# Performance work log

Hardware: AMD Instinct MI355X
Metric: run time of the kernel (lower is better)

## Reference

```python
import jax, jax.numpy as jnp
import numpy as np

N_NODES = 50000
N_EDGES = 800000
IN_C, HID_C, OUT_C, HEADS = 128, 32, 64, 8
NEG_SLOPE = 0.2


def gat_layer(x, src, dst, W, a_src, a_dst, bias, concat, num_nodes):
    # W: [F_in, H*C]; a_src, a_dst: [H, C]; bias: [H*C] or [C]
    H, C = a_src.shape
    h = (x @ W).reshape(num_nodes, H, C)                      # [N,H,C]
    e_src = (h * a_src).sum(-1)                               # [N,H]
    e_dst = (h * a_dst).sum(-1)                               # [N,H]
    e = jax.nn.leaky_relu(e_src[src] + e_dst[dst], NEG_SLOPE) # [E,H]
    # segment softmax over incoming edges of each destination node
    m = jax.ops.segment_max(e, dst, num_segments=num_nodes)   # [N,H]
    ex = jnp.exp(e - m[dst])
    den = jax.ops.segment_sum(ex, dst, num_segments=num_nodes)
    alpha = ex / (den[dst] + 1e-16)                           # [E,H]
    out = jax.ops.segment_sum(h[src] * alpha[..., None], dst, num_segments=num_nodes)  # [N,H,C]
    out = out.reshape(num_nodes, H * C) if concat else out.mean(axis=1)
    return out + bias


def setup_inputs() -> dict:
    key = jax.random.key(0)
    ks = jax.random.split(key, 10)
    x = jax.random.normal(ks[0], (N_NODES, IN_C), dtype=jnp.float32)
    edge_index = jax.random.randint(ks[1], (2, N_EDGES), 0, N_NODES, dtype=jnp.int64)
    s1 = (2.0 / (IN_C + HID_C * HEADS)) ** 0.5
    s2 = (2.0 / (HID_C * HEADS + OUT_C)) ** 0.5
    return {
        "x": x,
        "edge_index": edge_index,
        "W1": jax.random.normal(ks[2], (IN_C, HEADS * HID_C), dtype=jnp.float32) * s1,
        "a_src1": jax.random.normal(ks[3], (HEADS, HID_C), dtype=jnp.float32) * 0.1,
        "a_dst1": jax.random.normal(ks[4], (HEADS, HID_C), dtype=jnp.float32) * 0.1,
        "b1": jnp.zeros((HEADS * HID_C,), dtype=jnp.float32),
        "W2": jax.random.normal(ks[5], (HEADS * HID_C, OUT_C), dtype=jnp.float32) * s2,
        "a_src2": jax.random.normal(ks[6], (1, OUT_C), dtype=jnp.float32) * 0.1,
        "a_dst2": jax.random.normal(ks[7], (1, OUT_C), dtype=jnp.float32) * 0.1,
        "b2": jnp.zeros((OUT_C,), dtype=jnp.float32),
    }


def reference(x, edge_index, W1, a_src1, a_dst1, b1, W2, a_src2, a_dst2, b2):
    # add self-loops (PyG GATConv default)
    loops = jnp.arange(N_NODES, dtype=edge_index.dtype)
    src = jnp.concatenate([edge_index[0], loops])
    dst = jnp.concatenate([edge_index[1], loops])
    # dropout layers are identity in eval mode
    h = gat_layer(x, src, dst, W1, a_src1, a_dst1, b1, True, N_NODES)
    h = jax.nn.elu(h)
    out = gat_layer(h, src, dst, W2, a_src2, a_dst2, b2, False, N_NODES)
    return out
```

## Files before the change

kernel.cpp:

```cpp
#include <hip/hip_runtime.h>
#include <math.h>

#define N_NODES 50000
#define N_EDGES 800000
#define E_TOT   850000
#define IN_C    128
#define HID_C   32
#define OUT_C   64
#define HEADS   8
#define F1      256
#define PAD     64
#define NDUMMY  1024
#define G1_BLOCKS 3125
#define CSR_BLOCKS 782

typedef __bf16 bf16x8 __attribute__((ext_vector_type(8)));
typedef float  f32x4  __attribute__((ext_vector_type(4)));
typedef float  f32x2  __attribute__((ext_vector_type(2)));
typedef unsigned short us8 __attribute__((ext_vector_type(8)));

__device__ __forceinline__ unsigned short f2b(float f) {
    unsigned u = __float_as_uint(f);
    u += 0x7FFF + ((u >> 16) & 1);
    return (unsigned short)(u >> 16);
}
__device__ __forceinline__ float b2f(unsigned short b) {
    return __uint_as_float(((unsigned)b) << 16);
}
__device__ __forceinline__ float blo(unsigned u) { return __uint_as_float(u << 16); }
__device__ __forceinline__ float bhi(unsigned u) { return __uint_as_float(u & 0xffff0000u); }
__device__ __forceinline__ f32x2 up2(unsigned u) {
    f32x2 r; r.x = blo(u); r.y = bhi(u); return r;
}

__global__ void convert_w(const float* __restrict__ W1, const float* __restrict__ W2,
                          unsigned short* __restrict__ W1t, unsigned short* __restrict__ W2t,
                          int* __restrict__ deg, int* __restrict__ ssrc) {
    int gid = blockIdx.x * 256 + threadIdx.x;
    if (gid < N_NODES) {
        deg[gid] = 1;
        ssrc[gid * PAD] = gid;
    } else if (gid < N_NODES + NDUMMY) {
        deg[gid] = 0;
    }
    if (gid < 256 * 128) {
        int n = gid >> 7, k = gid & 127;
        W1t[gid] = f2b(W1[k * F1 + n]);
    } else if (gid < 256 * 128 + 64 * 256) {
        int o = gid - 256 * 128;
        int n = o >> 8, k = o & 255;
        W2t[o] = f2b(W2[k * OUT_C + n]);
    }
}

__global__ void csr_build(const int* __restrict__ ei, int* __restrict__ deg,
                          int* __restrict__ ssrc) {
    int e0 = blockIdx.x * 1024 + threadIdx.x;
    int s[4], d[4], p[4];
#pragma unroll
    for (int j = 0; j < 4; j++) {
        int e = e0 + j * 256;
        int le = (e < N_EDGES) ? e : (N_EDGES - 1);
        int es = ei[le];
        int ed = ei[N_EDGES + le];
        s[j] = es;
        d[j] = (e < N_EDGES) ? ed : (N_NODES + (e - N_EDGES));
    }
#pragma unroll
    for (int j = 0; j < 4; j++) p[j] = atomicAdd(&deg[d[j]], 1);
#pragma unroll
    for (int j = 0; j < 4; j++) ssrc[d[j] * PAD + p[j]] = s[j];
}

__global__ __launch_bounds__(256) void gemm1_mfma(const float* __restrict__ x,
                                                  const unsigned short* __restrict__ W1t,
                                                  const float* __restrict__ a_src,
                                                  const float* __restrict__ a_dst,
                                                  unsigned short* __restrict__ h1b,
                                                  float* __restrict__ e_src,
                                                  float* __restrict__ e_dst) {
    const int t = threadIdx.x;
    const int wave = t >> 6, lane = t & 63;
    const int mlane = lane & 15, quad = lane >> 4;
    const int row0 = blockIdx.x * 16;
    const int col0 = wave * 64;
    const float* xr = x + (size_t)(row0 + mlane) * IN_C;
    bf16x8 afr[4];
#pragma unroll
    for (int kc = 0; kc < 4; kc++) {
        float4 f0 = *(const float4*)&xr[kc * 32 + quad * 8];
        float4 f1 = *(const float4*)&xr[kc * 32 + quad * 8 + 4];
        us8 u;
        u[0] = f2b(f0.x); u[1] = f2b(f0.y); u[2] = f2b(f0.z); u[3] = f2b(f0.w);
        u[4] = f2b(f1.x); u[5] = f2b(f1.y); u[6] = f2b(f1.z); u[7] = f2b(f1.w);
        afr[kc] = __builtin_bit_cast(bf16x8, u);
    }
    f32x4 c[4];
#pragma unroll
    for (int nt = 0; nt < 4; nt++) c[nt] = (f32x4){0.f, 0.f, 0.f, 0.f};
#pragma unroll
    for (int kc = 0; kc < 4; kc++) {
#pragma unroll
        for (int nt = 0; nt < 4; nt++) {
            int col = col0 + nt * 16 + mlane;
            uint4 bw = *(const uint4*)&W1t[(size_t)col * IN_C + kc * 32 + quad * 8];
            bf16x8 b = __builtin_bit_cast(bf16x8, bw);
            c[nt] = __builtin_amdgcn_mfma_f32_16x16x32_bf16(afr[kc], b, c[nt], 0, 0, 0);
        }
    }
#pragma unroll
    for (int nt = 0; nt < 4; nt++) {
#pragma unroll
        for (int r = 0; r < 4; r++) {
            int gr = row0 + quad * 4 + r;
            h1b[(size_t)gr * F1 + col0 + nt * 16 + mlane] = f2b(c[nt][r]);
        }
    }
    float asA0 = a_src[col0 + mlane],      asA1 = a_src[col0 + 16 + mlane];
    float asB0 = a_src[col0 + 32 + mlane], asB1 = a_src[col0 + 48 + mlane];
    float adA0 = a_dst[col0 + mlane],      adA1 = a_dst[col0 + 16 + mlane];
    float adB0 = a_dst[col0 + 32 + mlane], adB1 = a_dst[col0 + 48 + mlane];
#pragma unroll
    for (int r = 0; r < 4; r++) {
        float psA = c[0][r] * asA0 + c[1][r] * asA1;
        float pdA = c[0][r] * adA0 + c[1][r] * adA1;
        float psB = c[2][r] * asB0 + c[3][r] * asB1;
        float pdB = c[2][r] * adB0 + c[3][r] * adB1;
#pragma unroll
        for (int off = 1; off < 16; off <<= 1) {
            psA += __shfl_xor(psA, off, 64);
            pdA += __shfl_xor(pdA, off, 64);
            psB += __shfl_xor(psB, off, 64);
            pdB += __shfl_xor(pdB, off, 64);
        }
        if (mlane == 0) {
            int gr = row0 + quad * 4 + r;
            e_src[gr * HEADS + wave * 2]     = psA;
            e_src[gr * HEADS + wave * 2 + 1] = psB;
            e_dst[gr * HEADS + wave * 2]     = pdA;
            e_dst[gr * HEADS + wave * 2 + 1] = pdB;
        }
    }
}

__global__ __launch_bounds__(256) void agg1s(const unsigned short* __restrict__ h1b,
                                             const float* __restrict__ e_src,
                                             const float* __restrict__ e_dst,
                                             const int* __restrict__ deg,
                                             const int* __restrict__ ssrc,
                                             const float* __restrict__ b1,
                                             unsigned short* __restrict__ hhb) {
    int v = (blockIdx.x * 256 + threadIdx.x) >> 6;
    int lane = threadIdx.x & 63;
    int half = lane >> 5, l32 = lane & 31;
    int c0 = l32 * 8, h_acc = l32 >> 2;
    int c2 = c0 << 1;
    int h_exp = l32 & 7, j_exp = l32 >> 3;
    const char* h1c = (const char*)h1b;
    const char* esc = (const char*)e_src;
    int d = deg[v];
    int beg = v * PAD;
    int s_all = ssrc[beg + lane];
    float edh = e_dst[v * HEADS + h_exp];
    f32x2 acc[4];
#pragma unroll
    for (int k = 0; k < 4; k++) acc[k] = (f32x2){0.f, 0.f};
    float den = 0.f;
    int dm1 = d - 1;
    for (int k16 = 0; k16 < d; k16 += 16) {
        int slotA = k16 + half + 2 * j_exp;
        int slotB = slotA + 8;
        int sA = __shfl(s_all, (slotA < dm1 ? slotA : dm1), 64);
        int sB = __shfl(s_all, (slotB < dm1 ? slotB : dm1), 64);
        float eA = *(const float*)(esc + ((sA << 5) + (h_exp << 2))) + edh;
        float eB = *(const float*)(esc + ((sB << 5) + (h_exp << 2))) + edh;
        eA = fmaxf(eA, 0.2f * eA);
        eB = fmaxf(eB, 0.2f * eB);
        float wA = (slotA < d) ? __expf(eA) : 0.f;
        float wB = (slotB < d) ? __expf(eB) : 0.f;
        int s_j[8];
#pragma unroll
        for (int j = 0; j < 8; j++) {
            int slot = k16 + half + 2 * j;
            s_j[j] = __shfl(s_all, (slot < dm1 ? slot : dm1), 64);
        }
        float w_j[8];
#pragma unroll
        for (int j = 0; j < 4; j++) {
            w_j[j]     = __shfl(wA, (j << 3) | h_acc, 32);
            w_j[j + 4] = __shfl(wB, (j << 3) | h_acc, 32);
        }
        uint4 r[8];
#pragma unroll
        for (int j = 0; j < 8; j++)
            r[j] = *(const uint4*)(h1c + (((unsigned)s_j[j] << 9) + c2));
#pragma unroll
        for (int j = 0; j < 8; j++) {
            den += w_j[j];
            acc[0] += w_j[j] * up2(r[j].x);
            acc[1] += w_j[j] * up2(r[j].y);
            acc[2] += w_j[j] * up2(r[j].z);
            acc[3] += w_j[j] * up2(r[j].w);
        }
    }
    den += __shfl_xor(den, 32, 64);
#pragma unroll
    for (int k = 0; k < 4; k++) {
        acc[k].x += __shfl_xor(acc[k].x, 32, 64);
        acc[k].y += __shfl_xor(acc[k].y, 32, 64);
    }
    if (half == 0) {
        float dinv = 1.f / (den + 1e-16f);
        us8 o;
#pragma unroll
        for (int k = 0; k < 4; k++) {
            float v0 = acc[k].x * dinv + b1[c0 + 2 * k];
            float v1 = acc[k].y * dinv + b1[c0 + 2 * k + 1];
            v0 = (v0 > 0.f) ? v0 : (__expf(v0) - 1.f);
            v1 = (v1 > 0.f) ? v1 : (__expf(v1) - 1.f);
            o[2 * k]     = f2b(v0);
            o[2 * k + 1] = f2b(v1);
        }
        *(us8*)&hhb[(size_t)v * F1 + c0] = o;
    }
}

__global__ __launch_bounds__(256) void gemm2_mfma(const unsigned short* __restrict__ hhb,
                                                  const unsigned short* __restrict__ W2t,
                                                  const float* __restrict__ a_src,
                                                  const float* __restrict__ a_dst,
                                                  unsigned short* __restrict__ h2b,
                                                  float* __restrict__ e_src,
                                                  float* __restrict__ e_dst) {
    const int t = threadIdx.x;
    const int wave = t >> 6, lane = t & 63;
    const int mlane = lane & 15, quad = lane >> 4;
    const int row0 = blockIdx.x * 64 + wave * 16;
    int arow = row0 + mlane;
    if (arow >= N_NODES) arow = N_NODES - 1;
    const unsigned short* ar = hhb + (size_t)arow * F1;
    f32x4 c[4];
#pragma unroll
    for (int nt = 0; nt < 4; nt++) c[nt] = (f32x4){0.f, 0.f, 0.f, 0.f};
#pragma unroll
    for (int kc = 0; kc < 8; kc++) {
        uint4 aw = *(const uint4*)&ar[kc * 32 + quad * 8];
        bf16x8 a = __builtin_bit_cast(bf16x8, aw);
#pragma unroll
        for (int nt = 0; nt < 4; nt++) {
            int col = nt * 16 + mlane;
            uint4 bw = *(const uint4*)&W2t[(size_t)col * F1 + kc * 32 + quad * 8];
            bf16x8 b = __builtin_bit_cast(bf16x8, bw);
            c[nt] = __builtin_amdgcn_mfma_f32_16x16x32_bf16(a, b, c[nt], 0, 0, 0);
        }
    }
#pragma unroll
    for (int nt = 0; nt < 4; nt++) {
#pragma unroll
        for (int r = 0; r < 4; r++) {
            int gr = row0 + quad * 4 + r;
            if (gr < N_NODES)
                h2b[(size_t)gr * OUT_C + nt * 16 + mlane] = f2b(c[nt][r]);
        }
    }
    float as0 = a_src[mlane],      as1 = a_src[16 + mlane];
    float as2 = a_src[32 + mlane], as3 = a_src[48 + mlane];
    float ad0 = a_dst[mlane],      ad1 = a_dst[16 + mlane];
    float ad2 = a_dst[32 + mlane], ad3 = a_dst[48 + mlane];
#pragma unroll
    for (int r = 0; r < 4; r++) {
        float ps = c[0][r] * as0 + c[1][r] * as1 + c[2][r] * as2 + c[3][r] * as3;
        float pd = c[0][r] * ad0 + c[1][r] * ad1 + c[2][r] * ad2 + c[3][r] * ad3;
#pragma unroll
        for (int off = 1; off < 16; off <<= 1) {
            ps += __shfl_xor(ps, off, 64);
            pd += __shfl_xor(pd, off, 64);
        }
        int gr = row0 + quad * 4 + r;
        if (mlane == 0 && gr < N_NODES) { e_src[gr] = ps; e_dst[gr] = pd; }
    }
}

__global__ __launch_bounds__(256) void agg2s(const unsigned short* __restrict__ h2b,
                                             const float* __restrict__ e_src,
                                             const float* __restrict__ e_dst,
                                             const int* __restrict__ deg,
                                             const int* __restrict__ ssrc,
                                             const float* __restrict__ b2,
                                             float* __restrict__ out) {
    int v = (blockIdx.x * 256 + threadIdx.x) >> 6;
    int lane = threadIdx.x & 63;
    int d = deg[v], beg = v * PAD, dm1 = d - 1;
    float ed = e_dst[v];
    int g = lane >> 3, l8 = lane & 7;
    int c0 = l8 * 8;
    int c2 = c0 << 1;
    const char* h2c = (const char*)h2b;
    const char* esc = (const char*)e_src;
    int s_raw = ssrc[beg + lane];
    int s_cl = s_raw < 0 ? 0 : (s_raw > N_NODES - 1 ? N_NODES - 1 : s_raw);
    float e_own = *(const float*)(esc + (s_cl << 2)) + ed;
    e_own = fmaxf(e_own, 0.2f * e_own);
    float w_own = (lane < d) ? __expf(e_own) : 0.f;
    f32x2 acc[4];
#pragma unroll
    for (int k = 0; k < 4; k++) acc[k] = (f32x2){0.f, 0.f};
    float den = 0.f;
    for (int k16 = 0; k16 < d; k16 += 16) {
        int slot0 = k16 + g, slot1 = slot0 + 8;
        int t0 = slot0 < dm1 ? slot0 : dm1;
        int t1 = slot1 < dm1 ? slot1 : dm1;
        int s0 = __shfl(s_cl, t0, 64);
        int s1 = __shfl(s_cl, t1, 64);
        float w0 = __shfl(w_own, t0, 64); w0 = (slot0 < d) ? w0 : 0.f;
        float w1 = __shfl(w_own, t1, 64); w1 = (slot1 < d) ? w1 : 0.f;
        den += w0 + w1;
        uint4 r0 = *(const uint4*)(h2c + ((s0 << 7) + c2));
        uint4 r1 = *(const uint4*)(h2c + ((s1 << 7) + c2));
        acc[0] += w0 * up2(r0.x) + w1 * up2(r1.x);
        acc[1] += w0 * up2(r0.y) + w1 * up2(r1.y);
        acc[2] += w0 * up2(r0.z) + w1 * up2(r1.z);
        acc[3] += w0 * up2(r0.w) + w1 * up2(r1.w);
    }
    den += __shfl_xor(den, 8, 64);
    den += __shfl_xor(den, 16, 64);
    den += __shfl_xor(den, 32, 64);
#pragma unroll
    for (int k = 0; k < 4; k++) {
        acc[k].x += __shfl_xor(acc[k].x, 8, 64);
        acc[k].y += __shfl_xor(acc[k].y, 8, 64);
        acc[k].x += __shfl_xor(acc[k].x, 16, 64);
        acc[k].y += __shfl_xor(acc[k].y, 16, 64);
        acc[k].x += __shfl_xor(acc[k].x, 32, 64);
        acc[k].y += __shfl_xor(acc[k].y, 32, 64);
    }
    if (g == 0) {
        float dinv = 1.f / (den + 1e-16f);
        float4 lo, hi;
        lo.x = acc[0].x * dinv + b2[c0 + 0]; lo.y = acc[0].y * dinv + b2[c0 + 1];
        lo.z = acc[1].x * dinv + b2[c0 + 2]; lo.w = acc[1].y * dinv + b2[c0 + 3];
        hi.x = acc[2].x * dinv + b2[c0 + 4]; hi.y = acc[2].y * dinv + b2[c0 + 5];
        hi.z = acc[3].x * dinv + b2[c0 + 6]; hi.w = acc[3].y * dinv + b2[c0 + 7];
        *(float4*)&out[(size_t)v * OUT_C + c0] = lo;
        *(float4*)&out[(size_t)v * OUT_C + c0 + 4] = hi;
    }
}

extern "C" void kernel_launch(void* const* d_in, const int* in_sizes, int n_in,
                              void* d_out, int out_size, void* d_ws, size_t ws_size,
                              hipStream_t stream) {
    const float* x      = (const float*)d_in[0];
    const int*   ei     = (const int*)d_in[1];
    const float* W1     = (const float*)d_in[2];
    const float* a_src1 = (const float*)d_in[3];
    const float* a_dst1 = (const float*)d_in[4];
    const float* b1     = (const float*)d_in[5];
    const float* W2     = (const float*)d_in[6];
    const float* a_src2 = (const float*)d_in[7];
    const float* a_dst2 = (const float*)d_in[8];
    const float* b2     = (const float*)d_in[9];
    float* out = (float*)d_out;

    char* ws = (char*)d_ws;
    size_t off = 0;
    auto alloc = [&](size_t bytes) { void* p = ws + off; off = (off + bytes + 255) & ~(size_t)255; return p; };
    unsigned short* h1b = (unsigned short*)alloc((size_t)N_NODES * F1 * 2);
    unsigned short* hhb = (unsigned short*)alloc((size_t)N_NODES * F1 * 2);
    unsigned short* h2b = (unsigned short*)alloc((size_t)N_NODES * OUT_C * 2);
    unsigned short* W1t = (unsigned short*)alloc((size_t)256 * 128 * 2);
    unsigned short* W2t = (unsigned short*)alloc((size_t)64 * 256 * 2);
    float* e_src1 = (float*)alloc((size_t)N_NODES * HEADS * 4);
    float* e_dst1 = (float*)alloc((size_t)N_NODES * HEADS * 4);
    float* e_src2 = (float*)alloc((size_t)N_NODES * 4);
    float* e_dst2 = (float*)alloc((size_t)N_NODES * 4);
    int*   deg    = (int*)alloc((size_t)(N_NODES + NDUMMY) * 4);
    int*   ssrc   = (int*)alloc((size_t)(N_NODES + NDUMMY) * PAD * 4);
    (void)ws_size; (void)n_in; (void)in_sizes; (void)out_size;

    const int g2_blocks  = (N_NODES + 63) / 64;
    const int node_waves = (N_NODES + 3) / 4;

    convert_w<<<200, 256, 0, stream>>>(W1, W2, W1t, W2t, deg, ssrc);
    csr_build<<<CSR_BLOCKS, 256, 0, stream>>>(ei, deg, ssrc);
    gemm1_mfma<<<G1_BLOCKS, 256, 0, stream>>>(x, W1t, a_src1, a_dst1, h1b, e_src1, e_dst1);
    agg1s<<<node_waves, 256, 0, stream>>>(h1b, e_src1, e_dst1, deg, ssrc, b1, hhb);
    gemm2_mfma<<<g2_blocks, 256, 0, stream>>>(hhb, W2t, a_src2, a_dst2, h2b, e_src2, e_dst2);
    agg2s<<<node_waves, 256, 0, stream>>>(h2b, e_src2, e_dst2, deg, ssrc, b2, out);
}
```

Before: 291.3 us.

## Fuse layer-2 linear transform into layer-1 aggregation kernel via LDS

The layer-1 aggregation kernel now keeps each node's ELU output row in shared memory and immediately multiplies it by W2 (repacked as bf16 pairs) with scalar FMAs. It also computes the layer-2 attention scores, so the separate MFMA GEMM2 kernel and the 25MB hhb intermediate buffer are removed. This saves a full write and read of the hidden activations plus one launch. In exchange, each wave now does a 256x64 dot product without tensor cores and reads W2 from cache per node. It also adds a __syncthreads inside the aggregation kernel.

```diff
diff --git a/kernel.cpp b/kernel.cpp
--- a/kernel.cpp
+++ b/kernel.cpp
@@ -34,7 +34,7 @@
 }
 
 __global__ void convert_w(const float* __restrict__ W1, const float* __restrict__ W2,
-                          unsigned short* __restrict__ W1t, unsigned short* __restrict__ W2t,
+                          unsigned short* __restrict__ W1t, unsigned* __restrict__ W2p,
                           int* __restrict__ deg, int* __restrict__ ssrc) {
     int gid = blockIdx.x * 256 + threadIdx.x;
     if (gid < N_NODES) {
@@ -46,10 +46,12 @@
     if (gid < 256 * 128) {
         int n = gid >> 7, k = gid & 127;
         W1t[gid] = f2b(W1[k * F1 + n]);
-    } else if (gid < 256 * 128 + 64 * 256) {
+    } else if (gid < 256 * 128 + 128 * 64) {
         int o = gid - 256 * 128;
-        int n = o >> 8, k = o & 255;
-        W2t[o] = f2b(W2[k * OUT_C + n]);
+        int kk = o >> 6, col = o & 63;
+        unsigned lo = f2b(W2[(2 * kk) * OUT_C + col]);
+        unsigned hi = f2b(W2[(2 * kk + 1) * OUT_C + col]);
+        W2p[o] = lo | (hi << 16);
     }
 }
 
@@ -143,14 +145,21 @@
     }
 }
 
-__global__ __launch_bounds__(256) void agg1s(const unsigned short* __restrict__ h1b,
+__global__ __launch_bounds__(256) void agg1f(const unsigned short* __restrict__ h1b,
                                              const float* __restrict__ e_src,
                                              const float* __restrict__ e_dst,
                                              const int* __restrict__ deg,
                                              const int* __restrict__ ssrc,
                                              const float* __restrict__ b1,
-                                             unsigned short* __restrict__ hhb) {
-    int v = (blockIdx.x * 256 + threadIdx.x) >> 6;
+                                             const unsigned* __restrict__ W2p,
+                                             const float* __restrict__ a_src2,
+                                             const float* __restrict__ a_dst2,
+                                             unsigned short* __restrict__ h2b,
+                                             float* __restrict__ e_src2,
+                                             float* __restrict__ e_dst2) {
+    __shared__ unsigned hh_lds[4][128];
+    int wave = threadIdx.x >> 6;
+    int v = blockIdx.x * 4 + wave;
     int lane = threadIdx.x & 63;
     int half = lane >> 5, l32 = lane & 31;
     int c0 = l32 * 8, h_acc = l32 >> 2;
@@ -221,64 +230,33 @@
             o[2 * k]     = f2b(v0);
             o[2 * k + 1] = f2b(v1);
         }
-        *(us8*)&hhb[(size_t)v * F1 + c0] = o;
-    }
-}
-
-__global__ __launch_bounds__(256) void gemm2_mfma(const unsigned short* __restrict__ hhb,
-                                                  const unsigned short* __restrict__ W2t,
-                                                  const float* __restrict__ a_src,
-                                                  const float* __restrict__ a_dst,
-                                                  unsigned short* __restrict__ h2b,
-                                                  float* __restrict__ e_src,
-                                                  float* __restrict__ e_dst) {
-    const int t = threadIdx.x;
-    const int wave = t >> 6, lane = t & 63;
-    const int mlane = lane & 15, quad = lane >> 4;
-    const int row0 = blockIdx.x * 64 + wave * 16;
-    int arow = row0 + mlane;
-    if (arow >= N_NODES) arow = N_NODES - 1;
-    const unsigned short* ar = hhb + (size_t)arow * F1;
-    f32x4 c[4];
-#pragma unroll
-    for (int nt = 0; nt < 4; nt++) c[nt] = (f32x4){0.f, 0.f, 0.f, 0.f};
-#pragma unroll
-    for (int kc = 0; kc < 8; kc++) {
-        uint4 aw = *(const uint4*)&ar[kc * 32 + quad * 8];
-        bf16x8 a = __builtin_bit_cast(bf16x8, aw);
-#pragma unroll
-        for (int nt = 0; nt < 4; nt++) {
-            int col = nt * 16 + mlane;
-            uint4 bw = *(const uint4*)&W2t[(size_t)col * F1 + kc * 32 + quad * 8];
-            bf16x8 b = __builtin_bit_cast(bf16x8, bw);
-            c[nt] = __builtin_amdgcn_mfma_f32_16x16x32_bf16(a, b, c[nt], 0, 0, 0);
-        }
-    }
-#pragma unroll
-    for (int nt = 0; nt < 4; nt++) {
-#pragma unroll
-        for (int r = 0; r < 4; r++) {
-            int gr = row0 + quad * 4 + r;
-            if (gr < N_NODES)
-                h2b[(size_t)gr * OUT_C + nt * 16 + mlane] = f2b(c[nt][r]);
-        }
-    }
-    float as0 = a_src[mlane],      as1 = a_src[16 + mlane];
-    float as2 = a_src[32 + mlane], as3 = a_src[48 + mlane];
-    float ad0 = a_dst[mlane],      ad1 = a_dst[16 + mlane];
-    float ad2 = a_dst[32 + mlane], ad3 = a_dst[48 + mlane];
-#pragma unroll
-    for (int r = 0; r < 4; r++) {
-        float ps = c[0][r] * as0 + c[1][r] * as1 + c[2][r] * as2 + c[3][r] * as3;
-        float pd = c[0][r] * ad0 + c[1][r] * ad1 + c[2][r] * ad2 + c[3][r] * ad3;
-#pragma unroll
-        for (int off = 1; off < 16; off <<= 1) {
-            ps += __shfl_xor(ps, off, 64);
-            pd += __shfl_xor(pd, off, 64);
-        }
-        int gr = row0 + quad * 4 + r;
-        if (mlane == 0 && gr < N_NODES) { e_src[gr] = ps; e_dst[gr] = pd; }
-    }
+        *(uint4*)&hh_lds[wave][l32 * 4] = __builtin_bit_cast(uint4, o);
+    }
+    __syncthreads();
+    const unsigned* hw = hh_lds[wave];
+    f32x2 macc = (f32x2){0.f, 0.f};
+#pragma unroll 4
+    for (int kk = 0; kk < 128; kk += 4) {
+        uint4 hv = *(const uint4*)&hw[kk];
+        unsigned w0 = W2p[(kk + 0) * 64 + lane];
+        unsigned w1 = W2p[(kk + 1) * 64 + lane];
+        unsigned w2 = W2p[(kk + 2) * 64 + lane];
+        unsigned w3 = W2p[(kk + 3) * 64 + lane];
+        macc += up2(hv.x) * up2(w0);
+        macc += up2(hv.y) * up2(w1);
+        macc += up2(hv.z) * up2(w2);
+        macc += up2(hv.w) * up2(w3);
+    }
+    float val = macc.x + macc.y;
+    h2b[(size_t)v * OUT_C + lane] = f2b(val);
+    float ps = val * a_src2[lane];
+    float pd = val * a_dst2[lane];
+#pragma unroll
+    for (int off = 1; off < 64; off <<= 1) {
+        ps += __shfl_xor(ps, off, 64);
+        pd += __shfl_xor(pd, off, 64);
+    }
+    if (lane == 0) { e_src2[v] = ps; e_dst2[v] = pd; }
 }
 
 __global__ __launch_bounds__(256) void agg2s(const unsigned short* __restrict__ h2b,
@@ -365,10 +343,9 @@
     size_t off = 0;
     auto alloc = [&](size_t bytes) { void* p = ws + off; off = (off + bytes + 255) & ~(size_t)255; return p; };
     unsigned short* h1b = (unsigned short*)alloc((size_t)N_NODES * F1 * 2);
-    unsigned short* hhb = (unsigned short*)alloc((size_t)N_NODES * F1 * 2);
     unsigned short* h2b = (unsigned short*)alloc((size_t)N_NODES * OUT_C * 2);
     unsigned short* W1t = (unsigned short*)alloc((size_t)256 * 128 * 2);
-    unsigned short* W2t = (unsigned short*)alloc((size_t)64 * 256 * 2);
+    unsigned*       W2p = (unsigned*)alloc((size_t)128 * 64 * 4);
     float* e_src1 = (float*)alloc((size_t)N_NODES * HEADS * 4);
     float* e_dst1 = (float*)alloc((size_t)N_NODES * HEADS * 4);
     float* e_src2 = (float*)alloc((size_t)N_NODES * 4);
@@ -377,13 +354,12 @@
     int*   ssrc   = (int*)alloc((size_t)(N_NODES + NDUMMY) * PAD * 4);
     (void)ws_size; (void)n_in; (void)in_sizes; (void)out_size;
 
-    const int g2_blocks  = (N_NODES + 63) / 64;
     const int node_waves = (N_NODES + 3) / 4;
 
-    convert_w<<<200, 256, 0, stream>>>(W1, W2, W1t, W2t, deg, ssrc);
+    convert_w<<<200, 256, 0, stream>>>(W1, W2, W1t, W2p, deg, ssrc);
     csr_build<<<CSR_BLOCKS, 256, 0, stream>>>(ei, deg, ssrc);
     gemm1_mfma<<<G1_BLOCKS, 256, 0, stream>>>(x, W1t, a_src1, a_dst1, h1b, e_src1, e_dst1);
-    agg1s<<<node_waves, 256, 0, stream>>>(h1b, e_src1, e_dst1, deg, ssrc, b1, hhb);
-    gemm2_mfma<<<g2_blocks, 256, 0, stream>>>(hhb, W2t, a_src2, a_dst2, h2b, e_src2, e_dst2);
+    agg1f<<<node_waves, 256, 0, stream>>>(h1b, e_src1, e_dst1, deg, ssrc, b1,
+                                          W2p, a_src2, a_dst2, h2b, e_src2, e_dst2);
     agg2s<<<node_waves, 256, 0, stream>>>(h2b, e_src2, e_dst2, deg, ssrc, b2, out);
 }
```

After: 316.1 us. 8.5% more time.

## Fuse layer-2 projection GEMM into layer-1 aggregation via shared memory

Applied to the files above, without the earlier changes.

The layer-1 aggregation kernel now writes its ELU'd bf16 output row into LDS instead of global memory. Each 4-node block then runs the 256x64 MFMA projection and the attention-logit reductions itself. This removes the 25.6 MB hhb round trip and one kernel launch. In exchange, each wave computes a 16-row MFMA tile of which only 4 rows are distinct nodes, W2 is reloaded per block, and a block-wide barrier now couples the four waves' variable-degree work.

```diff
diff --git a/kernel.cpp b/kernel.cpp
--- a/kernel.cpp
+++ b/kernel.cpp
@@ -143,14 +143,21 @@
     }
 }
 
-__global__ __launch_bounds__(256) void agg1s(const unsigned short* __restrict__ h1b,
+__global__ __launch_bounds__(256) void agg1f(const unsigned short* __restrict__ h1b,
                                              const float* __restrict__ e_src,
                                              const float* __restrict__ e_dst,
                                              const int* __restrict__ deg,
                                              const int* __restrict__ ssrc,
                                              const float* __restrict__ b1,
-                                             unsigned short* __restrict__ hhb) {
-    int v = (blockIdx.x * 256 + threadIdx.x) >> 6;
+                                             const unsigned short* __restrict__ W2t,
+                                             const float* __restrict__ a_src2,
+                                             const float* __restrict__ a_dst2,
+                                             unsigned short* __restrict__ h2b,
+                                             float* __restrict__ e_src2,
+                                             float* __restrict__ e_dst2) {
+    __shared__ unsigned hh_lds[4][128];
+    int wave = threadIdx.x >> 6;
+    int v = blockIdx.x * 4 + wave;
     int lane = threadIdx.x & 63;
     int half = lane >> 5, l32 = lane & 31;
     int c0 = l32 * 8, h_acc = l32 >> 2;
@@ -221,64 +228,47 @@
             o[2 * k]     = f2b(v0);
             o[2 * k + 1] = f2b(v1);
         }
-        *(us8*)&hhb[(size_t)v * F1 + c0] = o;
-    }
-}
-
-__global__ __launch_bounds__(256) void gemm2_mfma(const unsigned short* __restrict__ hhb,
-                                                  const unsigned short* __restrict__ W2t,
-                                                  const float* __restrict__ a_src,
-                                                  const float* __restrict__ a_dst,
-                                                  unsigned short* __restrict__ h2b,
-                                                  float* __restrict__ e_src,
-                                                  float* __restrict__ e_dst) {
-    const int t = threadIdx.x;
-    const int wave = t >> 6, lane = t & 63;
+        *(uint4*)&hh_lds[wave][l32 * 4] = __builtin_bit_cast(uint4, o);
+    }
+    __syncthreads();
     const int mlane = lane & 15, quad = lane >> 4;
-    const int row0 = blockIdx.x * 64 + wave * 16;
-    int arow = row0 + mlane;
-    if (arow >= N_NODES) arow = N_NODES - 1;
-    const unsigned short* ar = hhb + (size_t)arow * F1;
-    f32x4 c[4];
-#pragma unroll
-    for (int nt = 0; nt < 4; nt++) c[nt] = (f32x4){0.f, 0.f, 0.f, 0.f};
+    const unsigned short* hrow = (const unsigned short*)hh_lds[mlane & 3];
+    f32x4 cc[4];
+#pragma unroll
+    for (int nt = 0; nt < 4; nt++) cc[nt] = (f32x4){0.f, 0.f, 0.f, 0.f};
 #pragma unroll
     for (int kc = 0; kc < 8; kc++) {
-        uint4 aw = *(const uint4*)&ar[kc * 32 + quad * 8];
+        uint4 aw = *(const uint4*)&hrow[kc * 32 + quad * 8];
         bf16x8 a = __builtin_bit_cast(bf16x8, aw);
 #pragma unroll
         for (int nt = 0; nt < 4; nt++) {
             int col = nt * 16 + mlane;
             uint4 bw = *(const uint4*)&W2t[(size_t)col * F1 + kc * 32 + quad * 8];
             bf16x8 b = __builtin_bit_cast(bf16x8, bw);
-            c[nt] = __builtin_amdgcn_mfma_f32_16x16x32_bf16(a, b, c[nt], 0, 0, 0);
-        }
-    }
+            cc[nt] = __builtin_amdgcn_mfma_f32_16x16x32_bf16(a, b, cc[nt], 0, 0, 0);
+        }
+    }
+    float val[4];
 #pragma unroll
     for (int nt = 0; nt < 4; nt++) {
-#pragma unroll
-        for (int r = 0; r < 4; r++) {
-            int gr = row0 + quad * 4 + r;
-            if (gr < N_NODES)
-                h2b[(size_t)gr * OUT_C + nt * 16 + mlane] = f2b(c[nt][r]);
-        }
-    }
-    float as0 = a_src[mlane],      as1 = a_src[16 + mlane];
-    float as2 = a_src[32 + mlane], as3 = a_src[48 + mlane];
-    float ad0 = a_dst[mlane],      ad1 = a_dst[16 + mlane];
-    float ad2 = a_dst[32 + mlane], ad3 = a_dst[48 + mlane];
-#pragma unroll
-    for (int r = 0; r < 4; r++) {
-        float ps = c[0][r] * as0 + c[1][r] * as1 + c[2][r] * as2 + c[3][r] * as3;
-        float pd = c[0][r] * ad0 + c[1][r] * ad1 + c[2][r] * ad2 + c[3][r] * ad3;
-#pragma unroll
-        for (int off = 1; off < 16; off <<= 1) {
-            ps += __shfl_xor(ps, off, 64);
-            pd += __shfl_xor(pd, off, 64);
-        }
-        int gr = row0 + quad * 4 + r;
-        if (mlane == 0 && gr < N_NODES) { e_src[gr] = ps; e_dst[gr] = pd; }
-    }
+        float t0 = (wave & 1) ? cc[nt][1] : cc[nt][0];
+        float t1 = (wave & 1) ? cc[nt][3] : cc[nt][2];
+        val[nt] = (wave & 2) ? t1 : t0;
+    }
+    float ps = 0.f, pd = 0.f;
+#pragma unroll
+    for (int nt = 0; nt < 4; nt++) {
+        int col = nt * 16 + mlane;
+        if (quad == 0) h2b[(size_t)v * OUT_C + col] = f2b(val[nt]);
+        ps += val[nt] * a_src2[col];
+        pd += val[nt] * a_dst2[col];
+    }
+#pragma unroll
+    for (int off = 1; off < 16; off <<= 1) {
+        ps += __shfl_xor(ps, off, 64);
+        pd += __shfl_xor(pd, off, 64);
+    }
+    if (lane == 0) { e_src2[v] = ps; e_dst2[v] = pd; }
 }
 
 __global__ __launch_bounds__(256) void agg2s(const unsigned short* __restrict__ h2b,
@@ -365,7 +355,6 @@
     size_t off = 0;
     auto alloc = [&](size_t bytes) { void* p = ws + off; off = (off + bytes + 255) & ~(size_t)255; return p; };
     unsigned short* h1b = (unsigned short*)alloc((size_t)N_NODES * F1 * 2);
-    unsigned short* hhb = (unsigned short*)alloc((size_t)N_NODES * F1 * 2);
     unsigned short* h2b = (unsigned short*)alloc((size_t)N_NODES * OUT_C * 2);
     unsigned short* W1t = (unsigned short*)alloc((size_t)256 * 128 * 2);
     unsigned short* W2t = (unsigned short*)alloc((size_t)64 * 256 * 2);
@@ -377,13 +366,12 @@
     int*   ssrc   = (int*)alloc((size_t)(N_NODES + NDUMMY) * PAD * 4);
     (void)ws_size; (void)n_in; (void)in_sizes; (void)out_size;
 
-    const int g2_blocks  = (N_NODES + 63) / 64;
     const int node_waves = (N_NODES + 3) / 4;
 
     convert_w<<<200, 256, 0, stream>>>(W1, W2, W1t, W2t, deg, ssrc);
     csr_build<<<CSR_BLOCKS, 256, 0, stream>>>(ei, deg, ssrc);
     gemm1_mfma<<<G1_BLOCKS, 256, 0, stream>>>(x, W1t, a_src1, a_dst1, h1b, e_src1, e_dst1);
-    agg1s<<<node_waves, 256, 0, stream>>>(h1b, e_src1, e_dst1, deg, ssrc, b1, hhb);
-    gemm2_mfma<<<g2_blocks, 256, 0, stream>>>(hhb, W2t, a_src2, a_dst2, h2b, e_src2, e_dst2);
+    agg1f<<<node_waves, 256, 0, stream>>>(h1b, e_src1, e_dst1, deg, ssrc, b1,
+                                          W2t, a_src2, a_dst2, h2b, e_src2, e_dst2);
     agg2s<<<node_waves, 256, 0, stream>>>(h2b, e_src2, e_dst2, deg, ssrc, b2, out);
 }
```

After: 429.7 us. +47.5%, slower.

## Fold layer-2 attention projections into agg1 and restructure gemm2 tiling

Applied to the files above, without the earlier changes.

Precomputes W2·a_src2 and W2·a_dst2 once, then computes the layer-2 attention logits inside agg1s from the fp32 ELU outputs, which removes that reduction from gemm2. gemm2 is reorganised so each block handles 16 rows staged through shared memory, with each wave producing one 16-column slice. This gives more, smaller blocks. The logits now come from fp32 activations instead of bf16-rounded GEMM outputs, so numerics shift slightly.

```diff
diff --git a/kernel.cpp b/kernel.cpp
--- a/kernel.cpp
+++ b/kernel.cpp
@@ -34,7 +34,9 @@
 }
 
 __global__ void convert_w(const float* __restrict__ W1, const float* __restrict__ W2,
+                          const float* __restrict__ a_src2, const float* __restrict__ a_dst2,
                           unsigned short* __restrict__ W1t, unsigned short* __restrict__ W2t,
+                          float* __restrict__ w2s, float* __restrict__ w2d,
                           int* __restrict__ deg, int* __restrict__ ssrc) {
     int gid = blockIdx.x * 256 + threadIdx.x;
     if (gid < N_NODES) {
@@ -42,6 +44,15 @@
         ssrc[gid * PAD] = gid;
     } else if (gid < N_NODES + NDUMMY) {
         deg[gid] = 0;
+    }
+    if (gid < 256) {
+        float s = 0.f, dd = 0.f;
+        for (int c = 0; c < OUT_C; c++) {
+            float w = W2[gid * OUT_C + c];
+            s  += w * a_src2[c];
+            dd += w * a_dst2[c];
+        }
+        w2s[gid] = s; w2d[gid] = dd;
     }
     if (gid < 256 * 128) {
         int n = gid >> 7, k = gid & 127;
@@ -149,7 +160,11 @@
                                              const int* __restrict__ deg,
                                              const int* __restrict__ ssrc,
                                              const float* __restrict__ b1,
-                                             unsigned short* __restrict__ hhb) {
+                                             const float* __restrict__ w2s,
+                                             const float* __restrict__ w2d,
+                                             unsigned short* __restrict__ hhb,
+                                             float* __restrict__ e_src2,
+                                             float* __restrict__ e_dst2) {
     int v = (blockIdx.x * 256 + threadIdx.x) >> 6;
     int lane = threadIdx.x & 63;
     int half = lane >> 5, l32 = lane & 31;
@@ -212,6 +227,7 @@
     if (half == 0) {
         float dinv = 1.f / (den + 1e-16f);
         us8 o;
+        float ps = 0.f, pd = 0.f;
 #pragma unroll
         for (int k = 0; k < 4; k++) {
             float v0 = acc[k].x * dinv + b1[c0 + 2 * k];
@@ -220,64 +236,49 @@
             v1 = (v1 > 0.f) ? v1 : (__expf(v1) - 1.f);
             o[2 * k]     = f2b(v0);
             o[2 * k + 1] = f2b(v1);
+            ps += v0 * w2s[c0 + 2 * k] + v1 * w2s[c0 + 2 * k + 1];
+            pd += v0 * w2d[c0 + 2 * k] + v1 * w2d[c0 + 2 * k + 1];
         }
         *(us8*)&hhb[(size_t)v * F1 + c0] = o;
+#pragma unroll
+        for (int off = 1; off < 32; off <<= 1) {
+            ps += __shfl_xor(ps, off, 32);
+            pd += __shfl_xor(pd, off, 32);
+        }
+        if (l32 == 0) { e_src2[v] = ps; e_dst2[v] = pd; }
     }
 }
 
 __global__ __launch_bounds__(256) void gemm2_mfma(const unsigned short* __restrict__ hhb,
                                                   const unsigned short* __restrict__ W2t,
-                                                  const float* __restrict__ a_src,
-                                                  const float* __restrict__ a_dst,
-                                                  unsigned short* __restrict__ h2b,
-                                                  float* __restrict__ e_src,
-                                                  float* __restrict__ e_dst) {
+                                                  unsigned short* __restrict__ h2b) {
+    __shared__ unsigned short A[16 * 264];
     const int t = threadIdx.x;
     const int wave = t >> 6, lane = t & 63;
     const int mlane = lane & 15, quad = lane >> 4;
-    const int row0 = blockIdx.x * 64 + wave * 16;
-    int arow = row0 + mlane;
-    if (arow >= N_NODES) arow = N_NODES - 1;
-    const unsigned short* ar = hhb + (size_t)arow * F1;
-    f32x4 c[4];
-#pragma unroll
-    for (int nt = 0; nt < 4; nt++) c[nt] = (f32x4){0.f, 0.f, 0.f, 0.f};
+    const int row0 = blockIdx.x * 16;
+#pragma unroll
+    for (int i = 0; i < 2; i++) {
+        int u = t + i * 256;
+        int row = u >> 5, seg = u & 31;
+        uint4 w = *(const uint4*)&hhb[(size_t)(row0 + row) * F1 + seg * 8];
+        *(uint4*)&A[row * 264 + seg * 8] = w;
+    }
+    __syncthreads();
+    f32x4 cc = (f32x4){0.f, 0.f, 0.f, 0.f};
+    const int col = wave * 16 + mlane;
 #pragma unroll
     for (int kc = 0; kc < 8; kc++) {
-        uint4 aw = *(const uint4*)&ar[kc * 32 + quad * 8];
+        uint4 aw = *(const uint4*)&A[mlane * 264 + kc * 32 + quad * 8];
         bf16x8 a = __builtin_bit_cast(bf16x8, aw);
-#pragma unroll
-        for (int nt = 0; nt < 4; nt++) {
-            int col = nt * 16 + mlane;
-            uint4 bw = *(const uint4*)&W2t[(size_t)col * F1 + kc * 32 + quad * 8];
-            bf16x8 b = __builtin_bit_cast(bf16x8, bw);
-            c[nt] = __builtin_amdgcn_mfma_f32_16x16x32_bf16(a, b, c[nt], 0, 0, 0);
-        }
-    }
-#pragma unroll
-    for (int nt = 0; nt < 4; nt++) {
-#pragma unroll
-        for (int r = 0; r < 4; r++) {
-            int gr = row0 + quad * 4 + r;
-            if (gr < N_NODES)
-                h2b[(size_t)gr * OUT_C + nt * 16 + mlane] = f2b(c[nt][r]);
-        }
-    }
-    float as0 = a_src[mlane],      as1 = a_src[16 + mlane];
-    float as2 = a_src[32 + mlane], as3 = a_src[48 + mlane];
-    float ad0 = a_dst[mlane],      ad1 = a_dst[16 + mlane];
-    float ad2 = a_dst[32 + mlane], ad3 = a_dst[48 + mlane];
+        uint4 bw = *(const uint4*)&W2t[(size_t)col * F1 + kc * 32 + quad * 8];
+        bf16x8 b = __builtin_bit_cast(bf16x8, bw);
+        cc = __builtin_amdgcn_mfma_f32_16x16x32_bf16(a, b, cc, 0, 0, 0);
+    }
 #pragma unroll
     for (int r = 0; r < 4; r++) {
-        float ps = c[0][r] * as0 + c[1][r] * as1 + c[2][r] * as2 + c[3][r] * as3;
-        float pd = c[0][r] * ad0 + c[1][r] * ad1 + c[2][r] * ad2 + c[3][r] * ad3;
-#pragma unroll
-        for (int off = 1; off < 16; off <<= 1) {
-            ps += __shfl_xor(ps, off, 64);
-            pd += __shfl_xor(pd, off, 64);
-        }
         int gr = row0 + quad * 4 + r;
-        if (mlane == 0 && gr < N_NODES) { e_src[gr] = ps; e_dst[gr] = pd; }
+        h2b[(size_t)gr * OUT_C + wave * 16 + mlane] = f2b(cc[r]);
     }
 }
 
@@ -369,6 +370,8 @@
     unsigned short* h2b = (unsigned short*)alloc((size_t)N_NODES * OUT_C * 2);
     unsigned short* W1t = (unsigned short*)alloc((size_t)256 * 128 * 2);
     unsigned short* W2t = (unsigned short*)alloc((size_t)64 * 256 * 2);
+    float* w2s    = (float*)alloc((size_t)256 * 4);
+    float* w2d    = (float*)alloc((size_t)256 * 4);
     float* e_src1 = (float*)alloc((size_t)N_NODES * HEADS * 4);
     float* e_dst1 = (float*)alloc((size_t)N_NODES * HEADS * 4);
     float* e_src2 = (float*)alloc((size_t)N_NODES * 4);
@@ -377,13 +380,13 @@
     int*   ssrc   = (int*)alloc((size_t)(N_NODES + NDUMMY) * PAD * 4);
     (void)ws_size; (void)n_in; (void)in_sizes; (void)out_size;
 
-    const int g2_blocks  = (N_NODES + 63) / 64;
     const int node_waves = (N_NODES + 3) / 4;
 
-    convert_w<<<200, 256, 0, stream>>>(W1, W2, W1t, W2t, deg, ssrc);
+    convert_w<<<200, 256, 0, stream>>>(W1, W2, a_src2, a_dst2, W1t, W2t, w2s, w2d, deg, ssrc);
     csr_build<<<CSR_BLOCKS, 256, 0, stream>>>(ei, deg, ssrc);
     gemm1_mfma<<<G1_BLOCKS, 256, 0, stream>>>(x, W1t, a_src1, a_dst1, h1b, e_src1, e_dst1);
-    agg1s<<<node_waves, 256, 0, stream>>>(h1b, e_src1, e_dst1, deg, ssrc, b1, hhb);
-    gemm2_mfma<<<g2_blocks, 256, 0, stream>>>(hhb, W2t, a_src2, a_dst2, h2b, e_src2, e_dst2);
+    agg1s<<<node_waves, 256, 0, stream>>>(h1b, e_src1, e_dst1, deg, ssrc, b1,
+                                          w2s, w2d, hhb, e_src2, e_dst2);
+    gemm2_mfma<<<G1_BLOCKS, 256, 0, stream>>>(hhb, W2t, h2b);
     agg2s<<<node_waves, 256, 0, stream>>>(h2b, e_src2, e_dst2, deg, ssrc, b2, out);
 }
```

Result: no change. 288.6 us (-0.9%).
